# Kernel tuning notes

Measured on AMD Instinct MI355X. Metric: run time of the kernel, lower is better.

The kernel has to match this reference:

```python
import jax, jax.numpy as jnp
import numpy as np

N_U, N_M, E, H, L = 200000, 50000, 600000, 128, 2


def segment_mean(x, idx, n):
    s = jax.ops.segment_sum(x, idx, num_segments=n)
    d = jax.ops.segment_sum(jnp.ones((x.shape[0], 1), x.dtype), idx, num_segments=n)
    return s / jnp.maximum(d, 1.0)


def setup_inputs() -> dict:
    key = jax.random.key(0)
    ks = iter(jax.random.split(key, 40))
    g = lambda shape, scale: jax.random.normal(next(ks), shape, jnp.float32) * scale
    inp = {
        "user_x": g((N_U, 3), 1.0),
        "merchant_x": g((N_M, 2), 1.0),
        "edge_attr": g((E, 2), 1.0),
        "user_lin_w": g((3, H), 3 ** -0.5), "user_lin_b": jnp.zeros((H,), jnp.float32),
        "merchant_lin_w": g((2, H), 2 ** -0.5), "merchant_lin_b": jnp.zeros((H,), jnp.float32),
        "edge_lin_w": g((2, H), 2 ** -0.5), "edge_lin_b": jnp.zeros((H,), jnp.float32),
        # SAGEConv per layer, per relation: out = lin_l(mean_j x_j) + lin_r(x_dst)
        "conv_u2m_wl": g((L, H, H), H ** -0.5), "conv_u2m_bl": jnp.zeros((L, H), jnp.float32),
        "conv_u2m_wr": g((L, H, H), H ** -0.5),
        "conv_m2u_wl": g((L, H, H), H ** -0.5), "conv_m2u_bl": jnp.zeros((L, H), jnp.float32),
        "conv_m2u_wr": g((L, H, H), H ** -0.5),
        "c1_w": g((3 * H, H), (3 * H) ** -0.5), "c1_b": jnp.zeros((H,), jnp.float32),
        "c2_w": g((H, 1), H ** -0.5), "c2_b": jnp.zeros((1,), jnp.float32),
        "edge_index": jnp.stack([
            jax.random.randint(next(ks), (E,), 0, N_U),
            jax.random.randint(next(ks), (E,), 0, N_M),
        ]).astype(jnp.int64),
    }
    return inp


def reference(user_x, merchant_x, edge_attr,
              user_lin_w, user_lin_b, merchant_lin_w, merchant_lin_b,
              edge_lin_w, edge_lin_b,
              conv_u2m_wl, conv_u2m_bl, conv_u2m_wr,
              conv_m2u_wl, conv_m2u_bl, conv_m2u_wr,
              c1_w, c1_b, c2_w, c2_b, edge_index):
    relu = jax.nn.relu
    src, dst = edge_index[0], edge_index[1]  # user -> merchant

    h_u = relu(user_x @ user_lin_w + user_lin_b)        # [N_U, H]
    h_m = relu(merchant_x @ merchant_lin_w + merchant_lin_b)  # [N_M, H]
    e = relu(edge_attr @ edge_lin_w + edge_lin_b)       # [E, H]

    for l in range(L):
        # user -> merchant SAGEConv
        agg_m = segment_mean(h_u[src], dst, N_M)
        new_m = agg_m @ conv_u2m_wl[l] + conv_u2m_bl[l] + h_m @ conv_u2m_wr[l]
        # merchant -> user SAGEConv (reverse edges)
        agg_u = segment_mean(h_m[dst], src, N_U)
        new_u = agg_u @ conv_m2u_wl[l] + conv_m2u_bl[l] + h_u @ conv_m2u_wr[l]
        h_u, h_m = relu(new_u), relu(new_m)

    # vectorized form of the per-edge gather-concat-MLP loop
    feats = jnp.concatenate([h_u[src], h_m[dst], e], axis=-1)  # [E, 3H]
    hid = relu(feats @ c1_w + c1_b)  # dropout skipped (eval mode)
    out = hid @ c2_w + c2_b          # [E, 1]
    return out.squeeze(-1)           # [E]
```

## Files before the change

kernel.cpp:

```cpp
#include <hip/hip_runtime.h>

#define H   128
#define NU  200000
#define NM  50000
#define NE  600000

typedef __attribute__((ext_vector_type(8))) short bf16x8;
typedef __attribute__((ext_vector_type(4))) float f32x4;
typedef unsigned short ushort_t;
typedef unsigned int uint_t;

__device__ __forceinline__ ushort_t f2bf(float x) {
    uint_t b = __float_as_uint(x);
    return (ushort_t)((b + 0x7FFF + ((b >> 16) & 1)) >> 16);
}

__device__ __forceinline__ void gload16(const void* gsrc, void* lds_base) {
    __builtin_amdgcn_global_load_lds(
        (const __attribute__((address_space(1))) unsigned int*)gsrc,
        (__attribute__((address_space(3))) unsigned int*)lds_base,
        16, 0, 0);
}

__global__ void __launch_bounds__(256)
encode_bf16_kernel(const float* __restrict__ x, const float* __restrict__ W,
                   const float* __restrict__ b, ushort_t* __restrict__ h,
                   int n, int K) {
    int idx = blockIdx.x * 256 + threadIdx.x;
    if (idx >= n * 16) return;
    int r = idx >> 4, c0 = (idx & 15) * 8;
    float4 ba = *(const float4*)&b[c0], bb = *(const float4*)&b[c0 + 4];
    float acc[8] = {ba.x, ba.y, ba.z, ba.w, bb.x, bb.y, bb.z, bb.w};
    for (int k = 0; k < K; k++) {
        float xv = x[r * K + k];
        float4 wa = *(const float4*)&W[k * H + c0], wb = *(const float4*)&W[k * H + c0 + 4];
        acc[0] = fmaf(xv, wa.x, acc[0]); acc[1] = fmaf(xv, wa.y, acc[1]);
        acc[2] = fmaf(xv, wa.z, acc[2]); acc[3] = fmaf(xv, wa.w, acc[3]);
        acc[4] = fmaf(xv, wb.x, acc[4]); acc[5] = fmaf(xv, wb.y, acc[5]);
        acc[6] = fmaf(xv, wb.z, acc[6]); acc[7] = fmaf(xv, wb.w, acc[7]);
    }
    union { ushort_t u[8]; uint4 q; } pk;
#pragma unroll
    for (int j = 0; j < 8; j++) pk.u[j] = f2bf(fmaxf(acc[j], 0.f));
    *(uint4*)&h[(size_t)r * H + c0] = pk.q;
}

__global__ void count_kernel(const int* __restrict__ ei, int* cu, int* cm, int n) {
    int e = blockIdx.x * blockDim.x + threadIdx.x;
    if (e >= n) return;
    atomicAdd(&cu[ei[e]], 1);
    atomicAdd(&cm[ei[NE + e]], 1);
}

__global__ void __launch_bounds__(256)
scanA_kernel(const int* __restrict__ cnt, int* __restrict__ bsum, int n) {
    __shared__ int s[256];
    int b = blockIdx.x, t = threadIdx.x;
    int base = b * 2048 + t * 8;
    int sum = 0;
    if (base + 8 <= n) {
        int4 a = *(const int4*)&cnt[base];
        int4 c = *(const int4*)&cnt[base + 4];
        sum = a.x + a.y + a.z + a.w + c.x + c.y + c.z + c.w;
    } else {
        for (int j = 0; j < 8; j++) { int i = base + j; if (i < n) sum += cnt[i]; }
    }
    s[t] = sum;
    __syncthreads();
    for (int off = 128; off >= 1; off >>= 1) {
        if (t < off) s[t] += s[t + off];
        __syncthreads();
    }
    if (t == 0) bsum[b] = s[0];
}

__global__ void __launch_bounds__(256)
scanB_kernel(const int* __restrict__ bsum, int* __restrict__ boff, int nb,
             int* __restrict__ rp_total) {
    __shared__ int s[256];
    int t = threadIdx.x;
    int v = (t < nb) ? bsum[t] : 0;
    s[t] = v;
    __syncthreads();
    for (int off = 1; off < 256; off <<= 1) {
        int x = (t >= off) ? s[t - off] : 0;
        __syncthreads();
        s[t] += x;
        __syncthreads();
    }
    if (t < nb) boff[t] = s[t] - v;
    if (t == 255) rp_total[0] = s[255];
}

__global__ void __launch_bounds__(256)
scanC_kernel(const int* __restrict__ cnt, const int* __restrict__ boff,
             int* __restrict__ rp, int n) {
    __shared__ int s[256];
    int b = blockIdx.x, t = threadIdx.x;
    int base = b * 2048 + t * 8;
    int v[8];
    int sum = 0;
    if (base + 8 <= n) {
        int4 a = *(const int4*)&cnt[base];
        int4 c = *(const int4*)&cnt[base + 4];
        v[0] = a.x; v[1] = a.y; v[2] = a.z; v[3] = a.w;
        v[4] = c.x; v[5] = c.y; v[6] = c.z; v[7] = c.w;
#pragma unroll
        for (int j = 0; j < 8; j++) sum += v[j];
    } else {
#pragma unroll
        for (int j = 0; j < 8; j++) { int i = base + j; v[j] = (i < n) ? cnt[i] : 0; sum += v[j]; }
    }
    s[t] = sum;
    __syncthreads();
    for (int off = 1; off < 256; off <<= 1) {
        int x = (t >= off) ? s[t - off] : 0;
        __syncthreads();
        s[t] += x;
        __syncthreads();
    }
    int run = boff[b] + s[t] - sum;
    if (base + 8 <= n) {
        int o[8];
#pragma unroll
        for (int j = 0; j < 8; j++) { o[j] = run; run += v[j]; }
        *(int4*)&rp[base]     = make_int4(o[0], o[1], o[2], o[3]);
        *(int4*)&rp[base + 4] = make_int4(o[4], o[5], o[6], o[7]);
    } else {
#pragma unroll
        for (int j = 0; j < 8; j++) { int i = base + j; if (i < n) rp[i] = run; run += v[j]; }
    }
}

__global__ void fill_kernel(const int* __restrict__ ei, const int* __restrict__ rpu,
                            const int* __restrict__ rpm, int* cu, int* cm,
                            int* __restrict__ eu, int* __restrict__ em,
                            int* __restrict__ us, int* __restrict__ ue, int n) {
    int e = blockIdx.x * blockDim.x + threadIdx.x;
    if (e >= n) return;
    int s = ei[e], d = ei[NE + e];
    int slot = rpu[s] + atomicAdd(&cu[s], 1);
    eu[slot] = d;
    us[slot] = s;
    ue[slot] = e;
    em[rpm[d] + atomicAdd(&cm[d], 1)] = s;
}

__global__ void convert_w_kernel(const float* __restrict__ c1w, ushort_t* __restrict__ outT) {
    int i = blockIdx.x * 256 + threadIdx.x;
    if (i >= 384 * 128) return;
    int k = i >> 7, n = i & 127;
    outT[n * 384 + k] = f2bf(c1w[i]);
}

__global__ void convert_conv_w_kernel(const float* __restrict__ wl, const float* __restrict__ wr,
                                      ushort_t* __restrict__ outT) {
    int i = blockIdx.x * 256 + threadIdx.x;
    if (i >= 128 * 256) return;
    int col = i >> 8, k = i & 255;
    float v = (k < 128) ? wl[k * H + col] : wr[(k - 128) * H + col];
    outT[i] = f2bf(v);
}

__global__ void __launch_bounds__(512)
conv_pair_kernel(const ushort_t* __restrict__ hu_in, const ushort_t* __restrict__ hm_in,
                 const int* __restrict__ rpu, const int* __restrict__ rpm,
                 const int* __restrict__ eu, const int* __restrict__ em,
                 const ushort_t* __restrict__ wTm, const float* __restrict__ blm,
                 ushort_t* __restrict__ outM,
                 const ushort_t* __restrict__ wTu, const float* __restrict__ blu,
                 ushort_t* __restrict__ outU, int ntM) {
    const ushort_t *nbr, *self, *wT; const float* bl; ushort_t* out;
    const int *rp, *nbl; int n, tile;
    if ((int)blockIdx.x < ntM) {
        tile = blockIdx.x; nbr = hu_in; self = hm_in; rp = rpm; nbl = em;
        wT = wTm; bl = blm; out = outM; n = NM;
    } else {
        tile = blockIdx.x - ntM; nbr = hm_in; self = hu_in; rp = rpu; nbl = eu;
        wT = wTu; bl = blu; out = outU; n = NU;
    }
    int node0 = tile * 64;
    int t = threadIdx.x, lane = t & 63, w = t >> 6;
    int l15 = lane & 15, koff = lane >> 4;
    __shared__ ushort_t AsAgg[64 * 128];
    __shared__ ushort_t AsSelf[64 * 128];
    char* Aa = (char*)AsAgg;
    char* Asf = (char*)AsSelf;

#pragma unroll
    for (int it = 0; it < 2; it++) {
        int row = it * 32 + w * 4 + (lane >> 4);
        int node = node0 + row; if (node >= n) node = n - 1;
        int g = (lane & 15) ^ (row & 7);
        gload16(&self[(size_t)node * H + g * 8], Asf + it * 8192 + w * 1024);
    }

    for (int i = 0; i < 8; i++) {
        int row = w * 8 + i;
        int node = node0 + row;
        float a0 = 0.f, a1 = 0.f;
        int beg = 0, end = 0;
        if (node < n) { beg = rp[node]; end = rp[node + 1]; }
        int j = beg;
        for (; j + 4 <= end; j += 4) {
            int n0 = nbl[j], n1 = nbl[j + 1], n2 = nbl[j + 2], n3 = nbl[j + 3];
            uint_t v0 = *(const uint_t*)&nbr[(size_t)n0 * H + lane * 2];
            uint_t v1 = *(const uint_t*)&nbr[(size_t)n1 * H + lane * 2];
            uint_t v2 = *(const uint_t*)&nbr[(size_t)n2 * H + lane * 2];
            uint_t v3 = *(const uint_t*)&nbr[(size_t)n3 * H + lane * 2];
            a0 += (__uint_as_float((v0 & 0xffffu) << 16) + __uint_as_float((v1 & 0xffffu) << 16))
                + (__uint_as_float((v2 & 0xffffu) << 16) + __uint_as_float((v3 & 0xffffu) << 16));
            a1 += (__uint_as_float(v0 & 0xffff0000u) + __uint_as_float(v1 & 0xffff0000u))
                + (__uint_as_float(v2 & 0xffff0000u) + __uint_as_float(v3 & 0xffff0000u));
        }
        for (; j < end; j++) {
            uint_t v = *(const uint_t*)&nbr[(size_t)nbl[j] * H + lane * 2];
            a0 += __uint_as_float((v & 0xffffu) << 16);
            a1 += __uint_as_float(v & 0xffff0000u);
        }
        int deg = end - beg;
        float inv = 1.0f / (float)(deg > 1 ? deg : 1);
        uint_t r = (uint_t)f2bf(a0 * inv) | ((uint_t)f2bf(a1 * inv) << 16);
        *(uint_t*)(Aa + row * 256 + ((((lane >> 2)) ^ (row & 7)) << 4) + (lane & 3) * 4) = r;
    }

    bf16x8 bw[8];
    int col = w * 16 + l15;
#pragma unroll
    for (int ks = 0; ks < 8; ks++)
        bw[ks] = *reinterpret_cast<const bf16x8*>(&wT[col * 256 + ks * 32 + koff * 8]);
    float bias0 = bl[col];
    int sw = l15 & 7;
    __syncthreads();

    f32x4 acc[4];
#pragma unroll
    for (int rg = 0; rg < 4; rg++) acc[rg] = (f32x4){bias0, bias0, bias0, bias0};
#pragma unroll
    for (int ks = 0; ks < 8; ks++) {
#pragma unroll
        for (int rg = 0; rg < 4; rg++) {
            int row = rg * 16 + l15;
            const bf16x8 a = (ks < 4)
                ? *reinterpret_cast<const bf16x8*>(Aa  + row * 256 + (((ks * 4 + koff) ^ sw) << 4))
                : *reinterpret_cast<const bf16x8*>(Asf + row * 256 + ((((ks - 4) * 4 + koff) ^ sw) << 4));
            acc[rg] = __builtin_amdgcn_mfma_f32_16x16x32_bf16(a, bw[ks], acc[rg], 0, 0, 0);
        }
    }

#pragma unroll
    for (int rg = 0; rg < 4; rg++)
#pragma unroll
        for (int reg = 0; reg < 4; reg++) {
            int node = node0 + rg * 16 + koff * 4 + reg;
            if (node < n)
                out[(size_t)node * H + col] = f2bf(fmaxf(acc[rg][reg], 0.f));
        }
}

__global__ void __launch_bounds__(512)
edge_mlp_mfma_kernel(const ushort_t* __restrict__ h_u, const ushort_t* __restrict__ h_m,
                     const float* __restrict__ ea, const float* __restrict__ ew,
                     const float* __restrict__ ebias,
                     const ushort_t* __restrict__ c1wT, const float* __restrict__ c1b,
                     const float* __restrict__ c2w, const float* __restrict__ c2b,
                     const int* __restrict__ us, const int* __restrict__ eu,
                     const int* __restrict__ ue, float* __restrict__ out) {
    const int ET = 64;
    int nwg = gridDim.x;
    int q = nwg >> 3, r = nwg & 7;
    int xcd = blockIdx.x & 7, pos = blockIdx.x >> 3;
    int tile = (xcd < r ? xcd * (q + 1) : r * (q + 1) + (xcd - r) * q) + pos;
    int e0 = tile * ET;

    int t = threadIdx.x;
    int lane = t & 63, w = t >> 6;
    int l15 = lane & 15, koff = lane >> 4;

    __shared__ ushort_t As1[ET * 256];
    __shared__ ushort_t As2[ET * 128];
    __shared__ float part[8 * ET];
    __shared__ int se[ET], de[ET], ee[ET];
    char* Ab1 = (char*)As1;
    char* Ab2 = (char*)As2;

    if (t < ET) {
        se[t] = us[e0 + t];
        de[t] = eu[e0 + t];
        ee[t] = ue[e0 + t];
    }
    __syncthreads();

#pragma unroll
    for (int it = 0; it < 4; it++) {
        int row = it * 16 + w * 2 + (lane >> 5);
        int g = (lane & 31) ^ (row & 7);
        const ushort_t* src = (g < 16) ? &h_u[(size_t)se[row] * H + g * 8]
                                       : &h_m[(size_t)de[row] * H + (g - 16) * 8];
        gload16(src, Ab1 + it * 8192 + w * 1024);
    }

    bf16x8 bf_[12];
    int col = w * 16 + l15;
#pragma unroll
    for (int ks = 0; ks < 12; ks++)
        bf_[ks] = *reinterpret_cast<const bf16x8*>(&c1wT[col * 384 + ks * 32 + koff * 8]);

#pragma unroll
    for (int it = 0; it < 2; it++) {
        int lin = it * 512 + t;
        int row = lin >> 4, g2 = lin & 15;
        int c = g2 * 8;
        int eid = ee[row];
        float a0 = ea[(size_t)eid * 2], a1 = ea[(size_t)eid * 2 + 1];
        float4 w0a = *(const float4*)&ew[c];
        float4 w0b = *(const float4*)&ew[c + 4];
        float4 w1a = *(const float4*)&ew[H + c];
        float4 w1b = *(const float4*)&ew[H + c + 4];
        float4 bba = *(const float4*)&ebias[c];
        float4 bbb = *(const float4*)&ebias[c + 4];
        float v[8];
        v[0] = fmaxf(fmaf(a0, w0a.x, fmaf(a1, w1a.x, bba.x)), 0.f);
        v[1] = fmaxf(fmaf(a0, w0a.y, fmaf(a1, w1a.y, bba.y)), 0.f);
        v[2] = fmaxf(fmaf(a0, w0a.z, fmaf(a1, w1a.z, bba.z)), 0.f);
        v[3] = fmaxf(fmaf(a0, w0a.w, fmaf(a1, w1a.w, bba.w)), 0.f);
        v[4] = fmaxf(fmaf(a0, w0b.x, fmaf(a1, w1b.x, bbb.x)), 0.f);
        v[5] = fmaxf(fmaf(a0, w0b.y, fmaf(a1, w1b.y, bbb.y)), 0.f);
        v[6] = fmaxf(fmaf(a0, w0b.z, fmaf(a1, w1b.z, bbb.z)), 0.f);
        v[7] = fmaxf(fmaf(a0, w0b.w, fmaf(a1, w1b.w, bbb.w)), 0.f);
        union { ushort_t u[8]; uint4 q; } pk;
#pragma unroll
        for (int j = 0; j < 8; j++) pk.u[j] = f2bf(v[j]);
        *(uint4*)(Ab2 + row * 256 + ((g2 ^ (row & 7)) << 4)) = pk.q;
    }
    __syncthreads();

    int sw = l15 & 7;
    float bias0 = c1b[col];
    f32x4 acc[4];
#pragma unroll
    for (int rg = 0; rg < 4; rg++) acc[rg] = (f32x4){bias0, bias0, bias0, bias0};
#pragma unroll
    for (int ks = 0; ks < 12; ks++) {
#pragma unroll
        for (int rg = 0; rg < 4; rg++) {
            int row = rg * 16 + l15;
            const bf16x8 a = (ks < 8)
                ? *reinterpret_cast<const bf16x8*>(Ab1 + row * 512 + (((ks * 4 + koff) ^ sw) << 4))
                : *reinterpret_cast<const bf16x8*>(Ab2 + row * 256 + ((((ks - 8) * 4 + koff) ^ sw) << 4));
            acc[rg] = __builtin_amdgcn_mfma_f32_16x16x32_bf16(a, bf_[ks], acc[rg], 0, 0, 0);
        }
    }

    float c2v = c2w[col];
#pragma unroll
    for (int rg = 0; rg < 4; rg++) {
#pragma unroll
        for (int reg = 0; reg < 4; reg++) {
            float p = fmaxf(acc[rg][reg], 0.f) * c2v;
#pragma unroll
            for (int off = 8; off >= 1; off >>= 1) p += __shfl_xor(p, off, 64);
            if (l15 == 0) part[w * ET + rg * 16 + koff * 4 + reg] = p;
        }
    }
    __syncthreads();
    if (t < ET) {
        float s = part[t];
#pragma unroll
        for (int ww = 1; ww < 8; ww++) s += part[ww * ET + t];
        out[ee[t]] = s + c2b[0];
    }
}

extern "C" void kernel_launch(void* const* d_in, const int* in_sizes, int n_in,
                              void* d_out, int out_size, void* d_ws, size_t ws_size,
                              hipStream_t stream) {
    const float* user_x     = (const float*)d_in[0];
    const float* merchant_x = (const float*)d_in[1];
    const float* edge_attr  = (const float*)d_in[2];
    const float* user_w     = (const float*)d_in[3];
    const float* user_b     = (const float*)d_in[4];
    const float* merch_w    = (const float*)d_in[5];
    const float* merch_b    = (const float*)d_in[6];
    const float* edge_w     = (const float*)d_in[7];
    const float* edge_b     = (const float*)d_in[8];
    const float* u2m_wl     = (const float*)d_in[9];
    const float* u2m_bl     = (const float*)d_in[10];
    const float* u2m_wr     = (const float*)d_in[11];
    const float* m2u_wl     = (const float*)d_in[12];
    const float* m2u_bl     = (const float*)d_in[13];
    const float* m2u_wr     = (const float*)d_in[14];
    const float* c1w        = (const float*)d_in[15];
    const float* c1b        = (const float*)d_in[16];
    const float* c2w        = (const float*)d_in[17];
    const float* c2b        = (const float*)d_in[18];
    const int*   ei         = (const int*)d_in[19];
    float* out = (float*)d_out;

    ushort_t* hu   = (ushort_t*)d_ws;
    ushort_t* hm   = hu  + (size_t)NU * H;
    ushort_t* hu2  = hm  + (size_t)NM * H;
    ushort_t* hm2  = hu2 + (size_t)NU * H;
    ushort_t* c1wT = hm2 + (size_t)NM * H;
    ushort_t* wTc  = c1wT + 384 * 128;
    int* rpu = (int*)(wTc + 4 * 128 * 256);
    int* rpm = rpu + (NU + 1);
    int* cu  = rpm + (NM + 1);
    int* cm  = cu + NU;
    int* eu  = cm + NM;
    int* em  = eu + NE;
    int* us  = em + NE;
    int* ue  = us + NE;
    int* bsum_u = ue + NE;
    int* boff_u = bsum_u + 128;
    int* bsum_m = boff_u + 128;
    int* boff_m = bsum_m + 128;

    const int NBU = (NU + 2047) / 2048;
    const int NBM = (NM + 2047) / 2048;

    hipMemsetAsync(cu, 0, (size_t)(NU + NM) * sizeof(int), stream);

    encode_bf16_kernel<<<(NU * 16 + 255) / 256, 256, 0, stream>>>(user_x, user_w, user_b, hu, NU, 3);
    encode_bf16_kernel<<<(NM * 16 + 255) / 256, 256, 0, stream>>>(merchant_x, merch_w, merch_b, hm, NM, 2);
    convert_w_kernel<<<(384 * 128 + 255) / 256, 256, 0, stream>>>(c1w, c1wT);
    for (int l = 0; l < 2; l++) {
        convert_conv_w_kernel<<<128, 256, 0, stream>>>(
            u2m_wl + (size_t)l * H * H, u2m_wr + (size_t)l * H * H, wTc + (size_t)l * 128 * 256);
        convert_conv_w_kernel<<<128, 256, 0, stream>>>(
            m2u_wl + (size_t)l * H * H, m2u_wr + (size_t)l * H * H, wTc + (size_t)(2 + l) * 128 * 256);
    }

    count_kernel<<<(NE + 255) / 256, 256, 0, stream>>>(ei, cu, cm, NE);
    scanA_kernel<<<NBU, 256, 0, stream>>>(cu, bsum_u, NU);
    scanB_kernel<<<1, 256, 0, stream>>>(bsum_u, boff_u, NBU, rpu + NU);
    scanC_kernel<<<NBU, 256, 0, stream>>>(cu, boff_u, rpu, NU);
    scanA_kernel<<<NBM, 256, 0, stream>>>(cm, bsum_m, NM);
    scanB_kernel<<<1, 256, 0, stream>>>(bsum_m, boff_m, NBM, rpm + NM);
    scanC_kernel<<<NBM, 256, 0, stream>>>(cm, boff_m, rpm, NM);
    hipMemsetAsync(cu, 0, (size_t)(NU + NM) * sizeof(int), stream);
    fill_kernel<<<(NE + 255) / 256, 256, 0, stream>>>(ei, rpu, rpm, cu, cm, eu, em, us, ue, NE);

    const int CONV_TILES_M = (NM + 63) / 64;
    const int CONV_TILES_U = (NU + 63) / 64;

    const ushort_t* pu = hu; const ushort_t* pm = hm;
    ushort_t* qu = hu2; ushort_t* qm = hm2;
    for (int l = 0; l < 2; l++) {
        conv_pair_kernel<<<CONV_TILES_M + CONV_TILES_U, 512, 0, stream>>>(
            pu, pm, rpu, rpm, eu, em,
            wTc + (size_t)l * 128 * 256, u2m_bl + (size_t)l * H, qm,
            wTc + (size_t)(2 + l) * 128 * 256, m2u_bl + (size_t)l * H, qu,
            CONV_TILES_M);
        const ushort_t* tu = pu; pu = qu; qu = (ushort_t*)tu;
        const ushort_t* tm = pm; pm = qm; qm = (ushort_t*)tm;
    }

    edge_mlp_mfma_kernel<<<NE / 64, 512, 0, stream>>>(pu, pm, edge_attr, edge_w, edge_b,
                                                      c1wT, c1b, c2w, c2b, us, eu, ue, out);
}
```

Measured before the change: 580.1 us.

## Dedup user rows per edge tile, pre-permute edge attrs, fragment-order weight layout

The edge MLP kernel now finds runs of identical source users among the 64 CSR-sorted edges of a tile. It gathers each unique user row into LDS only once and indexes it per edge, which cuts redundant global gathers. Edge attributes are permuted into slot order inside fill_kernel, so the edge kernel reads them contiguously instead of through the ee indirection. The converted weights are stored in MFMA fragment order so each lane's B-fragment load is coalesced. In exchange the kernel adds a wave-level scan, an extra workspace buffer, and a data-dependent loop count.

```diff
diff --git a/kernel.cpp b/kernel.cpp
--- a/kernel.cpp
+++ b/kernel.cpp
@@ -135,7 +135,8 @@
 __global__ void fill_kernel(const int* __restrict__ ei, const int* __restrict__ rpu,
                             const int* __restrict__ rpm, int* cu, int* cm,
                             int* __restrict__ eu, int* __restrict__ em,
-                            int* __restrict__ us, int* __restrict__ ue, int n) {
+                            int* __restrict__ us, int* __restrict__ ue,
+                            const float* __restrict__ ea, float* __restrict__ eas, int n) {
     int e = blockIdx.x * blockDim.x + threadIdx.x;
     if (e >= n) return;
     int s = ei[e], d = ei[NE + e];
@@ -143,21 +144,28 @@
     eu[slot] = d;
     us[slot] = s;
     ue[slot] = e;
+    *(float2*)&eas[(size_t)slot * 2] = *(const float2*)&ea[(size_t)e * 2];
     em[rpm[d] + atomicAdd(&cm[d], 1)] = s;
 }
 
 __global__ void convert_w_kernel(const float* __restrict__ c1w, ushort_t* __restrict__ outT) {
     int i = blockIdx.x * 256 + threadIdx.x;
     if (i >= 384 * 128) return;
-    int k = i >> 7, n = i & 127;
-    outT[n * 384 + k] = f2bf(c1w[i]);
+    int j = i & 7, chunk = i >> 3;
+    int l15 = chunk & 15, koff = (chunk >> 4) & 3, wks = chunk >> 6;
+    int ks = wks % 12, w = wks / 12;
+    int col = w * 16 + l15, k = ks * 32 + koff * 8 + j;
+    outT[i] = f2bf(c1w[k * H + col]);
 }
 
 __global__ void convert_conv_w_kernel(const float* __restrict__ wl, const float* __restrict__ wr,
                                       ushort_t* __restrict__ outT) {
     int i = blockIdx.x * 256 + threadIdx.x;
     if (i >= 128 * 256) return;
-    int col = i >> 8, k = i & 255;
+    int j = i & 7, chunk = i >> 3;
+    int l15 = chunk & 15, koff = (chunk >> 4) & 3, wks = chunk >> 6;
+    int ks = wks & 7, w = wks >> 3;
+    int col = w * 16 + l15, k = ks * 32 + koff * 8 + j;
     float v = (k < 128) ? wl[k * H + col] : wr[(k - 128) * H + col];
     outT[i] = f2bf(v);
 }
@@ -225,10 +233,11 @@
     }
 
     bf16x8 bw[8];
+#pragma unroll
+    for (int ks = 0; ks < 8; ks++)
+        bw[ks] = *reinterpret_cast<const bf16x8*>(
+            &wT[(size_t)((((w * 8 + ks) * 4 + koff) * 16 + l15)) * 8]);
     int col = w * 16 + l15;
-#pragma unroll
-    for (int ks = 0; ks < 8; ks++)
-        bw[ks] = *reinterpret_cast<const bf16x8*>(&wT[col * 256 + ks * 32 + koff * 8]);
     float bias0 = bl[col];
     int sw = l15 & 7;
     __syncthreads();
@@ -260,7 +269,7 @@
 
 __global__ void __launch_bounds__(512)
 edge_mlp_mfma_kernel(const ushort_t* __restrict__ h_u, const ushort_t* __restrict__ h_m,
-                     const float* __restrict__ ea, const float* __restrict__ ew,
+                     const float* __restrict__ eas, const float* __restrict__ ew,
                      const float* __restrict__ ebias,
                      const ushort_t* __restrict__ c1wT, const float* __restrict__ c1b,
                      const float* __restrict__ c2w, const float* __restrict__ c2b,
@@ -277,42 +286,63 @@
     int lane = t & 63, w = t >> 6;
     int l15 = lane & 15, koff = lane >> 4;
 
-    __shared__ ushort_t As1[ET * 256];
+    __shared__ ushort_t Uh[ET * 128];
+    __shared__ ushort_t Mh[ET * 128];
     __shared__ ushort_t As2[ET * 128];
     __shared__ float part[8 * ET];
-    __shared__ int se[ET], de[ET], ee[ET];
-    char* Ab1 = (char*)As1;
+    __shared__ int de[ET], ee[ET], uid_s[ET], ulist_s[ET];
+    __shared__ int nuniq_s;
+    char* Ub = (char*)Uh;
+    char* Mb = (char*)Mh;
     char* Ab2 = (char*)As2;
 
     if (t < ET) {
-        se[t] = us[e0 + t];
+        int sv = us[e0 + t];
         de[t] = eu[e0 + t];
         ee[t] = ue[e0 + t];
-    }
-    __syncthreads();
-
-#pragma unroll
-    for (int it = 0; it < 4; it++) {
-        int row = it * 16 + w * 2 + (lane >> 5);
-        int g = (lane & 31) ^ (row & 7);
-        const ushort_t* src = (g < 16) ? &h_u[(size_t)se[row] * H + g * 8]
-                                       : &h_m[(size_t)de[row] * H + (g - 16) * 8];
-        gload16(src, Ab1 + it * 8192 + w * 1024);
+        int prev = __shfl_up(sv, 1, 64);
+        int flag = (t > 0 && sv != prev) ? 1 : 0;
+        int scan = flag;
+#pragma unroll
+        for (int off = 1; off < 64; off <<= 1) {
+            int v = __shfl_up(scan, off, 64);
+            if (t >= off) scan += v;
+        }
+        uid_s[t] = scan;
+        if (flag || t == 0) ulist_s[scan] = sv;
+        if (t == 63) nuniq_s = scan + 1;
+    }
+    __syncthreads();
+
+    int nuniq = nuniq_s;
+
+    int rounds = (nuniq + 31) >> 5;
+    for (int it = 0; it < rounds; it++) {
+        int urow = it * 32 + w * 4 + (lane >> 4);
+        if (urow < nuniq) {
+            int g = (lane & 15) ^ (urow & 7);
+            gload16(&h_u[(size_t)ulist_s[urow] * H + g * 8], Ub + it * 8192 + w * 1024);
+        }
+    }
+#pragma unroll
+    for (int it = 0; it < 2; it++) {
+        int mrow = it * 32 + w * 4 + (lane >> 4);
+        int g = (lane & 15) ^ (mrow & 7);
+        gload16(&h_m[(size_t)de[mrow] * H + g * 8], Mb + it * 8192 + w * 1024);
     }
 
     bf16x8 bf_[12];
-    int col = w * 16 + l15;
 #pragma unroll
     for (int ks = 0; ks < 12; ks++)
-        bf_[ks] = *reinterpret_cast<const bf16x8*>(&c1wT[col * 384 + ks * 32 + koff * 8]);
+        bf_[ks] = *reinterpret_cast<const bf16x8*>(
+            &c1wT[(size_t)((((w * 12 + ks) * 4 + koff) * 16 + l15)) * 8]);
 
 #pragma unroll
     for (int it = 0; it < 2; it++) {
         int lin = it * 512 + t;
         int row = lin >> 4, g2 = lin & 15;
         int c = g2 * 8;
-        int eid = ee[row];
-        float a0 = ea[(size_t)eid * 2], a1 = ea[(size_t)eid * 2 + 1];
+        float a0 = eas[(size_t)(e0 + row) * 2], a1 = eas[(size_t)(e0 + row) * 2 + 1];
         float4 w0a = *(const float4*)&ew[c];
         float4 w0b = *(const float4*)&ew[c + 4];
         float4 w1a = *(const float4*)&ew[H + c];
@@ -328,14 +358,20 @@
         v[5] = fmaxf(fmaf(a0, w0b.y, fmaf(a1, w1b.y, bbb.y)), 0.f);
         v[6] = fmaxf(fmaf(a0, w0b.z, fmaf(a1, w1b.z, bbb.z)), 0.f);
         v[7] = fmaxf(fmaf(a0, w0b.w, fmaf(a1, w1b.w, bbb.w)), 0.f);
-        union { ushort_t u[8]; uint4 q; } pk;
+        union { ushort_t u[8]; uint4 qq; } pk;
 #pragma unroll
         for (int j = 0; j < 8; j++) pk.u[j] = f2bf(v[j]);
-        *(uint4*)(Ab2 + row * 256 + ((g2 ^ (row & 7)) << 4)) = pk.q;
-    }
+        *(uint4*)(Ab2 + row * 256 + ((g2 ^ (row & 7)) << 4)) = pk.qq;
+    }
+
+    int uidr[4];
+#pragma unroll
+    for (int rg = 0; rg < 4; rg++) uidr[rg] = uid_s[rg * 16 + l15];
+
     __syncthreads();
 
     int sw = l15 & 7;
+    int col = w * 16 + l15;
     float bias0 = c1b[col];
     f32x4 acc[4];
 #pragma unroll
@@ -345,9 +381,14 @@
 #pragma unroll
         for (int rg = 0; rg < 4; rg++) {
             int row = rg * 16 + l15;
-            const bf16x8 a = (ks < 8)
-                ? *reinterpret_cast<const bf16x8*>(Ab1 + row * 512 + (((ks * 4 + koff) ^ sw) << 4))
-                : *reinterpret_cast<const bf16x8*>(Ab2 + row * 256 + ((((ks - 8) * 4 + koff) ^ sw) << 4));
+            const bf16x8 a = (ks < 4)
+                ? *reinterpret_cast<const bf16x8*>(
+                      Ub + uidr[rg] * 256 + ((((ks * 4 + koff) ^ (uidr[rg] & 7))) << 4))
+                : (ks < 8)
+                ? *reinterpret_cast<const bf16x8*>(
+                      Mb + row * 256 + ((((ks - 4) * 4 + koff) ^ sw) << 4))
+                : *reinterpret_cast<const bf16x8*>(
+                      Ab2 + row * 256 + ((((ks - 8) * 4 + koff) ^ sw) << 4));
             acc[rg] = __builtin_amdgcn_mfma_f32_16x16x32_bf16(a, bf_[ks], acc[rg], 0, 0, 0);
         }
     }
@@ -411,7 +452,8 @@
     int* em  = eu + NE;
     int* us  = em + NE;
     int* ue  = us + NE;
-    int* bsum_u = ue + NE;
+    float* eas = (float*)(ue + NE);
+    int* bsum_u = (int*)(eas + 2 * (size_t)NE);
     int* boff_u = bsum_u + 128;
     int* bsum_m = boff_u + 128;
     int* boff_m = bsum_m + 128;
@@ -439,7 +481,8 @@
     scanB_kernel<<<1, 256, 0, stream>>>(bsum_m, boff_m, NBM, rpm + NM);
     scanC_kernel<<<NBM, 256, 0, stream>>>(cm, boff_m, rpm, NM);
     hipMemsetAsync(cu, 0, (size_t)(NU + NM) * sizeof(int), stream);
-    fill_kernel<<<(NE + 255) / 256, 256, 0, stream>>>(ei, rpu, rpm, cu, cm, eu, em, us, ue, NE);
+    fill_kernel<<<(NE + 255) / 256, 256, 0, stream>>>(ei, rpu, rpm, cu, cm, eu, em, us, ue,
+                                                      edge_attr, eas, NE);
 
     const int CONV_TILES_M = (NM + 63) / 64;
     const int CONV_TILES_U = (NU + 63) / 64;
@@ -456,6 +499,6 @@
         const ushort_t* tm = pm; pm = qm; qm = (ushort_t*)tm;
     }
 
-    edge_mlp_mfma_kernel<<<NE / 64, 512, 0, stream>>>(pu, pm, edge_attr, edge_w, edge_b,
+    edge_mlp_mfma_kernel<<<NE / 64, 512, 0, stream>>>(pu, pm, eas, edge_w, edge_b,
                                                       c1wT, c1b, c2w, c2b, us, eu, ue, out);
 }
```

Measured after the change: 525.9 us, median of 2. -9.4%, faster.
